# Optimization experiments

Hardware: AMD Instinct MI355X
Metric: run time of the kernel (lower is better)

## Reference

```python
import jax, jax.numpy as jnp
import numpy as np

B, H, T, D = 4, 16, 1024, 64
N_BINS = 16
TEMPERATURE = 1.0
THRESHOLD = 0.05
ROUTER_HIDDEN = 128


def setup_inputs() -> dict:
    key = jax.random.key(0)
    ks = jax.random.split(key, 7)
    key_dim = H * D
    return {
        "q": jax.random.normal(ks[0], (B, H, T, D), dtype=jnp.float32),
        "k": jax.random.normal(ks[1], (B, H, T, D), dtype=jnp.float32),
        "v": jax.random.normal(ks[2], (B, H, T, D), dtype=jnp.float32),
        "W1": jax.random.normal(ks[3], (key_dim, ROUTER_HIDDEN), dtype=jnp.float32) * (1.0 / np.sqrt(key_dim)),
        "b1": jnp.zeros((ROUTER_HIDDEN,), dtype=jnp.float32),
        "W2": jax.random.normal(ks[4], (ROUTER_HIDDEN, N_BINS), dtype=jnp.float32) * (1.0 / np.sqrt(ROUTER_HIDDEN)),
        "b2": jnp.zeros((N_BINS,), dtype=jnp.float32),
    }


def reference(q, k, v, W1, b1, W2, b2):
    b, h, t, d = q.shape
    # Router operates on keys flattened across heads: [B, T, H*D]
    k_flat = jnp.transpose(k, (0, 2, 1, 3)).reshape(b, t, h * d)
    hidden = jnp.tanh(k_flat @ W1 + b1)
    bucket_logits = hidden @ W2 + b2                      # [B, T, n_bins]
    bucket_probs = jax.nn.softmax(bucket_logits / TEMPERATURE, axis=-1)
    # Pairwise bucket similarity: [B, T, T]
    bucket_sim = jnp.einsum('bik,bjk->bij', bucket_probs, bucket_probs)
    bucket_mask = bucket_sim > THRESHOLD
    causal = jnp.tril(jnp.ones((t, t), dtype=bool))
    mask = causal[None, :, :] & bucket_mask               # [B, T, T]
    scale = d ** (-0.5)
    scores = jnp.einsum('bhtd,bhsd->bhts', q, k) * scale  # [B, H, T, T]
    scores = jnp.where(mask[:, None, :, :], scores, -jnp.inf)
    attn = jax.nn.softmax(scores, axis=-1)
    return jnp.einsum('bhts,bhsd->bhtd', attn, v)
```

## Files before the change

### kernel.cpp

```cpp
#include <hip/hip_runtime.h>
#include <hip/hip_bf16.h>


#define B_ 4
#define H_ 16
#define T_ 1024
#define D_ 64
#define NB 16
#define RH 128

typedef __attribute__((ext_vector_type(8))) short s16x8;
typedef __attribute__((ext_vector_type(4))) float f32x4;

__device__ __forceinline__ unsigned short f2bf(float x) {
  union { __hip_bfloat16 b; unsigned short u; } c;
  c.b = __hip_bfloat16(x);
  return c.u;
}
__device__ __forceinline__ float bf2f(unsigned short h) {
  return __uint_as_float(((unsigned)h) << 16);
}

__global__ __launch_bounds__(256) void router_v2(
    const float* __restrict__ kin, const float* __restrict__ W1,
    const float* __restrict__ b1, const float* __restrict__ W2,
    const float* __restrict__ b2, float* __restrict__ probs) {
  __shared__ float rows[8][1024];
  __shared__ float part[8][8][RH];
  __shared__ float hid[8][RH + 4];
  __shared__ float logits[8][NB];

  const int tid = threadIdx.x;
  const int bb = blockIdx.x;
  const int b = bb >> 7;
  const int t0 = (bb & 127) << 3;

#pragma unroll
  for (int s = 0; s < 8; s++) {
    const int idx4 = tid + 256 * s;
    const int r = idx4 >> 8, i = (idx4 & 255) * 4;
    const int h = i >> 6, d = i & 63;
    *(float4*)&rows[r][i] =
        *(const float4*)&kin[(((size_t)(b * H_) + h) * T_ + (t0 + r)) * D_ + d];
  }
  __syncthreads();

  const int hu0 = (tid & 31) << 2;
  const int k0 = (tid >> 5) << 7;
  float acc[8][4];
#pragma unroll
  for (int r = 0; r < 8; r++)
#pragma unroll
    for (int c = 0; c < 4; c++) acc[r][c] = 0.0f;

  for (int kb = 0; kb < 128; kb += 4) {
    float4 rv[8];
#pragma unroll
    for (int r = 0; r < 8; r++) rv[r] = *(const float4*)&rows[r][k0 + kb];
#pragma unroll
    for (int e = 0; e < 4; e++) {
      const float4 w = *(const float4*)&W1[(size_t)(k0 + kb + e) * RH + hu0];
#pragma unroll
      for (int r = 0; r < 8; r++) {
        const float rx = (&rv[r].x)[e];
        acc[r][0] += rx * w.x; acc[r][1] += rx * w.y;
        acc[r][2] += rx * w.z; acc[r][3] += rx * w.w;
      }
    }
  }
#pragma unroll
  for (int r = 0; r < 8; r++)
    *(float4*)&part[tid >> 5][r][hu0] =
        (float4){acc[r][0], acc[r][1], acc[r][2], acc[r][3]};
  __syncthreads();

  {
    const int p0 = tid * 4;
    const int r = p0 >> 7, hu = p0 & 127;
    float4 s = {0.f, 0.f, 0.f, 0.f};
#pragma unroll
    for (int sl = 0; sl < 8; sl++) {
      const float4 v = *(const float4*)&part[sl][r][hu];
      s.x += v.x; s.y += v.y; s.z += v.z; s.w += v.w;
    }
    const float4 bv = *(const float4*)&b1[hu];
    *(float4*)&hid[r][hu] = (float4){tanhf(s.x + bv.x), tanhf(s.y + bv.y),
                                     tanhf(s.z + bv.z), tanhf(s.w + bv.w)};
  }
  __syncthreads();

  if (tid < 128) {
    const int r = tid >> 4, bin = tid & 15;
    float a = b2[bin];
#pragma unroll
    for (int jj = 0; jj < RH; jj++) a += hid[r][jj] * W2[jj * NB + bin];
    logits[r][bin] = a;
  }
  __syncthreads();

  if (tid < 8) {
    const int r = tid;
    float mx = -INFINITY;
#pragma unroll
    for (int bin = 0; bin < NB; bin++) mx = fmaxf(mx, logits[r][bin]);
    float e[NB];
    float s = 0.0f;
#pragma unroll
    for (int bin = 0; bin < NB; bin++) {
      e[bin] = expf(logits[r][bin] - mx);
      s += e[bin];
    }
    const float inv = 1.0f / s;
    const size_t row = (size_t)(b * T_ + t0 + r) * NB;
#pragma unroll
    for (int bin = 0; bin < NB; bin++) probs[row + bin] = e[bin] * inv;
  }
}

__global__ __launch_bounds__(256) void mask_v3(
    const float* __restrict__ probs, unsigned long long* __restrict__ mask) {
  const int blk = blockIdx.x;
  const int b = blk >> 7, i0 = (blk & 127) << 3;
  const int tid = threadIdx.x, w = tid >> 6;

  float4 pjv[4][4];
#pragma unroll
  for (int jc = 0; jc < 4; jc++) {
    const float4* pjp =
        (const float4*)(probs + ((size_t)(b * T_ + jc * 256 + tid)) * NB);
#pragma unroll
    for (int qq = 0; qq < 4; qq++) pjv[jc][qq] = pjp[qq];
  }

  for (int ii = 0; ii < 8; ii++) {
    const int i = i0 + ii;
    const float4* pip = (const float4*)(probs + ((size_t)(b * T_ + i)) * NB);
    const float4 p0 = pip[0], p1 = pip[1], p2 = pip[2], p3 = pip[3];
#pragma unroll
    for (int jc = 0; jc < 4; jc++) {
      const int j = jc * 256 + tid;
      float sim = p0.x * pjv[jc][0].x + p0.y * pjv[jc][0].y +
                  p0.z * pjv[jc][0].z + p0.w * pjv[jc][0].w;
      sim += p1.x * pjv[jc][1].x + p1.y * pjv[jc][1].y +
             p1.z * pjv[jc][1].z + p1.w * pjv[jc][1].w;
      sim += p2.x * pjv[jc][2].x + p2.y * pjv[jc][2].y +
             p2.z * pjv[jc][2].z + p2.w * pjv[jc][2].w;
      sim += p3.x * pjv[jc][3].x + p3.y * pjv[jc][3].y +
             p3.z * pjv[jc][3].z + p3.w * pjv[jc][3].w;
      const unsigned long long bal = __ballot((j <= i) && (sim > 0.05f));
      if ((tid & 63) == 0)
        mask[((size_t)(b * T_ + i) << 4) + jc * 4 + w] = bal;
    }
  }
}

__global__ __launch_bounds__(256, 2) void attn_mfma(
    const float* __restrict__ q, const float* __restrict__ k,
    const float* __restrict__ v, const unsigned long long* __restrict__ mask,
    float* __restrict__ out) {
  __shared__ unsigned short Kh[64 * 64], Kl[64 * 64];
  __shared__ unsigned short Vth[64 * 64], Vtl[64 * 64];
  __shared__ unsigned short Phs[4][1024], Pls[4][1024];

  const int bh = blockIdx.x, qt = blockIdx.y;
  const int b = bh >> 4;
  const int tid = threadIdx.x, w = tid >> 6, lane = tid & 63;
  const int lr = lane & 15;
  const int g = lane >> 4;
  const size_t base = (size_t)bh * (T_ * D_);
  const int qrow_g = qt * 64 + w * 16 + lr;
  const unsigned swz = ((unsigned)(lr & 7)) << 4;

  s16x8 qfh[2], qfl[2];
  {
    const float* qp = q + base + (size_t)qrow_g * D_;
#pragma unroll
    for (int ks = 0; ks < 2; ks++) {
      union { unsigned short us[8]; s16x8 v; } h, l;
#pragma unroll
      for (int e2 = 0; e2 < 2; e2++) {
        const float4 f = *(const float4*)(qp + 32 * ks + 8 * g + 4 * e2);
#pragma unroll
        for (int e = 0; e < 4; e++) {
          const float x = (&f.x)[e] * 0.125f;
          const unsigned short hh = f2bf(x);
          h.us[4 * e2 + e] = hh;
          l.us[4 * e2 + e] = f2bf(x - bf2f(hh));
        }
      }
      qfh[ks] = h.v; qfl[ks] = l.v;
    }
  }

  f32x4 Oacc[4];
#pragma unroll
  for (int n = 0; n < 4; n++) Oacc[n] = (f32x4){0.f, 0.f, 0.f, 0.f};
  float mrun = -INFINITY, lrun = 0.f;

  const unsigned long long* mrow = mask + ((size_t)(b * T_ + qrow_g) << 4);
  const int dv = tid & 63, k0v = (tid >> 6) * 16;

  float Kst[16], Vst[16], Kst2[16], Vst2[16];
  {
    const float4* kp4 = (const float4*)(k + base);
    const float* vp = v + base;
#pragma unroll
    for (int i = 0; i < 4; i++) {
      const float4 f = kp4[tid + 256 * i];
      Kst[4 * i + 0] = f.x; Kst[4 * i + 1] = f.y;
      Kst[4 * i + 2] = f.z; Kst[4 * i + 3] = f.w;
    }
#pragma unroll
    for (int j = 0; j < 16; j++) Vst[j] = vp[(size_t)(k0v + j) * D_ + dv];
  }
  unsigned long long mw = mrow[0];

  for (int kt = 0; kt <= qt; kt++) {
    __syncthreads();
#pragma unroll
    for (int i = 0; i < 4; i++) {
      const int flat4 = tid + 256 * i, key = flat4 >> 4, dq = flat4 & 15;
      union { unsigned short us[4]; uint2 d; } h, l;
#pragma unroll
      for (int e = 0; e < 4; e++) {
        const float x = Kst[4 * i + e];
        const unsigned short hh = f2bf(x);
        h.us[e] = hh; l.us[e] = f2bf(x - bf2f(hh));
      }
      const unsigned byte = (unsigned)(key * 128 + dq * 8) ^ (((unsigned)(key & 7)) << 4);
      *(uint2*)((char*)Kh + byte) = h.d;
      *(uint2*)((char*)Kl + byte) = l.d;
    }
#pragma unroll
    for (int i = 0; i < 2; i++) {
      union { unsigned short us[8]; uint4 q; } h, l;
#pragma unroll
      for (int j = 0; j < 8; j++) {
        const float x = Vst[8 * i + j];
        const unsigned short hh = f2bf(x);
        h.us[j] = hh; l.us[j] = f2bf(x - bf2f(hh));
      }
      const unsigned byte =
          (unsigned)(dv * 128 + (k0v + 8 * i) * 2) ^ (((unsigned)(dv & 7)) << 4);
      *(uint4*)((char*)Vth + byte) = h.q;
      *(uint4*)((char*)Vtl + byte) = l.q;
    }
    __syncthreads();

    const int ktn = (kt < qt) ? kt + 1 : qt;
    {
      const float4* kp4 = (const float4*)(k + base + (size_t)(ktn * 64) * D_);
      const float* vp = v + base + (size_t)(ktn * 64) * D_;
#pragma unroll
      for (int i = 0; i < 4; i++) {
        const float4 f = kp4[tid + 256 * i];
        Kst2[4 * i + 0] = f.x; Kst2[4 * i + 1] = f.y;
        Kst2[4 * i + 2] = f.z; Kst2[4 * i + 3] = f.w;
      }
#pragma unroll
      for (int j = 0; j < 16; j++) Vst2[j] = vp[(size_t)(k0v + j) * D_ + dv];
    }
    const unsigned long long mwn = mrow[ktn];

    if (__any(mw != 0ull)) {
      f32x4 S4[4];
#pragma unroll
      for (int m = 0; m < 4; m++) {
        f32x4 acc = (f32x4){0.f, 0.f, 0.f, 0.f};
#pragma unroll
        for (int ks = 0; ks < 2; ks++) {
          const unsigned byte =
              ((unsigned)((16 * m + lr) * 128 + 64 * ks + 16 * g)) ^ swz;
          const s16x8 kfh = *(const s16x8*)((const char*)Kh + byte);
          const s16x8 kfl = *(const s16x8*)((const char*)Kl + byte);
          acc = __builtin_amdgcn_mfma_f32_16x16x32_bf16(kfh, qfh[ks], acc, 0, 0, 0);
          acc = __builtin_amdgcn_mfma_f32_16x16x32_bf16(kfh, qfl[ks], acc, 0, 0, 0);
          acc = __builtin_amdgcn_mfma_f32_16x16x32_bf16(kfl, qfh[ks], acc, 0, 0, 0);
        }
        S4[m] = acc;
      }

      float sv[16]; unsigned okb = 0; float tmax = -INFINITY;
#pragma unroll
      for (int jj = 0; jj < 16; jj++) {
        const int bit = 16 * (jj >> 2) + 4 * g + (jj & 3);
        const bool ok = (mw >> bit) & 1ull;
        okb |= ((unsigned)ok) << jj;
        const float s = ok ? S4[jj >> 2][jj & 3] : -INFINITY;
        sv[jj] = s; tmax = fmaxf(tmax, s);
      }
      tmax = fmaxf(tmax, __shfl_xor(tmax, 16));
      tmax = fmaxf(tmax, __shfl_xor(tmax, 32));
      if (__any(tmax > mrun + 8.0f)) {
        const float mnew = fmaxf(mrun, tmax);
        const float corr = (mnew == -INFINITY) ? 1.0f : __expf(mrun - mnew);
        lrun *= corr; mrun = mnew;
        float cr[4];
#pragma unroll
        for (int r = 0; r < 4; r++) cr[r] = __shfl(corr, 4 * g + r);
#pragma unroll
        for (int n = 0; n < 4; n++)
#pragma unroll
          for (int r = 0; r < 4; r++) Oacc[n][r] *= cr[r];
      }
      float pj[16]; float lsum = 0.f;
#pragma unroll
      for (int jj = 0; jj < 16; jj++) {
        const float e = __expf(sv[jj] - mrun);
        const float pv = ((okb >> jj) & 1u) ? e : 0.f;
        pj[jj] = pv; lsum += pv;
      }
      lsum += __shfl_xor(lsum, 16);
      lsum += __shfl_xor(lsum, 32);
      lrun += lsum;

#pragma unroll
      for (int m = 0; m < 4; m++) {
        union { unsigned short us[4]; uint2 d; } h, l;
#pragma unroll
        for (int r = 0; r < 4; r++) {
          const float pv = pj[4 * m + r];
          const unsigned short hh = f2bf(pv);
          h.us[r] = hh; l.us[r] = f2bf(pv - bf2f(hh));
        }
        const unsigned byte =
            ((unsigned)(lr * 128 + (16 * m + 4 * g) * 2)) ^ swz;
        *(uint2*)((char*)Phs + 2048 * w + byte) = h.d;
        *(uint2*)((char*)Pls + 2048 * w + byte) = l.d;
      }
      asm volatile("s_waitcnt lgkmcnt(0)" ::: "memory");
      __builtin_amdgcn_sched_barrier(0);

#pragma unroll
      for (int ks = 0; ks < 2; ks++) {
        const unsigned pb = ((unsigned)(lr * 128 + 64 * ks + 16 * g)) ^ swz;
        const s16x8 pfh = *(const s16x8*)((const char*)Phs + 2048 * w + pb);
        const s16x8 pfl = *(const s16x8*)((const char*)Pls + 2048 * w + pb);
#pragma unroll
        for (int n = 0; n < 4; n++) {
          const unsigned vb =
              ((unsigned)((16 * n + lr) * 128 + 64 * ks + 16 * g)) ^ swz;
          const s16x8 vfh = *(const s16x8*)((const char*)Vth + vb);
          const s16x8 vfl = *(const s16x8*)((const char*)Vtl + vb);
          Oacc[n] = __builtin_amdgcn_mfma_f32_16x16x32_bf16(pfh, vfh, Oacc[n], 0, 0, 0);
          Oacc[n] = __builtin_amdgcn_mfma_f32_16x16x32_bf16(pfh, vfl, Oacc[n], 0, 0, 0);
          Oacc[n] = __builtin_amdgcn_mfma_f32_16x16x32_bf16(pfl, vfh, Oacc[n], 0, 0, 0);
        }
      }
    }

#pragma unroll
    for (int i = 0; i < 16; i++) { Kst[i] = Kst2[i]; Vst[i] = Vst2[i]; }
    mw = mwn;
  }

  const float linv = 1.0f / lrun;
  float lr4[4];
#pragma unroll
  for (int r = 0; r < 4; r++) lr4[r] = __shfl(linv, 4 * g + r);
  const int orow0 = qt * 64 + w * 16;
  float* op = out + base;
#pragma unroll
  for (int n = 0; n < 4; n++)
#pragma unroll
    for (int r = 0; r < 4; r++)
      op[(size_t)(orow0 + 4 * g + r) * D_ + 16 * n + lr] = Oacc[n][r] * lr4[r];
}

extern "C" void kernel_launch(void* const* d_in, const int* in_sizes, int n_in,
                              void* d_out, int out_size, void* d_ws, size_t ws_size,
                              hipStream_t stream) {
  const float* q  = (const float*)d_in[0];
  const float* k  = (const float*)d_in[1];
  const float* v  = (const float*)d_in[2];
  const float* W1 = (const float*)d_in[3];
  const float* b1 = (const float*)d_in[4];
  const float* W2 = (const float*)d_in[5];
  const float* b2 = (const float*)d_in[6];
  float* out = (float*)d_out;

  float* probs = (float*)d_ws;
  unsigned long long* mask =
      (unsigned long long*)((char*)d_ws + (size_t)B_ * T_ * NB * sizeof(float));

  router_v2<<<512, 256, 0, stream>>>(k, W1, b1, W2, b2, probs);
  mask_v3<<<512, 256, 0, stream>>>(probs, mask);
  attn_mfma<<<dim3(B_ * H_, T_ / 64), 256, 0, stream>>>(q, k, v, mask, out);
}
```

Measured before the change: 170.2 us.

## Pre-split K/V into swizzled bf16 hi/lo tiles and reorder attention blocks

The router kernel gains extra blocks that convert K and transposed V once into bf16 hi/lo pairs, stored in workspace in the swizzled LDS layout. The attention kernel then copies these tiles straight into shared memory with register double-buffering, instead of converting fp32 K/V in every query-tile block. It also launches heaviest causal query tiles first, skips fully masked tiles, only rescales the accumulator when the running max grows by more than a margin, and drops the low part of P. The cost is 32 MB of extra workspace traffic plus a fallback path when the workspace is too small, and less precision in the P·V product.

```diff
diff --git a/kernel.cpp b/kernel.cpp
--- a/kernel.cpp
+++ b/kernel.cpp
@@ -21,99 +21,160 @@
   return __uint_as_float(((unsigned)h) << 16);
 }
 
-__global__ __launch_bounds__(256) void router_v2(
-    const float* __restrict__ kin, const float* __restrict__ W1,
-    const float* __restrict__ b1, const float* __restrict__ W2,
-    const float* __restrict__ b2, float* __restrict__ probs) {
-  __shared__ float rows[8][1024];
-  __shared__ float part[8][8][RH];
-  __shared__ float hid[8][RH + 4];
-  __shared__ float logits[8][NB];
-
+__global__ __launch_bounds__(256) void prep_kernel(
+    const float* __restrict__ kin, const float* __restrict__ vin,
+    const float* __restrict__ W1, const float* __restrict__ b1,
+    const float* __restrict__ W2, const float* __restrict__ b2,
+    float* __restrict__ probs,
+    unsigned short* __restrict__ khi, unsigned short* __restrict__ klo,
+    unsigned short* __restrict__ vthi, unsigned short* __restrict__ vtlo) {
+  __shared__ union {
+    struct {
+      float rows[8][1024];
+      float part[8][8][RH];
+      float hid[8][RH + 4];
+      float logits[8][NB];
+    } r;
+    float vt[64][68];
+  } sm;
   const int tid = threadIdx.x;
-  const int bb = blockIdx.x;
-  const int b = bb >> 7;
-  const int t0 = (bb & 127) << 3;
-
-#pragma unroll
-  for (int s = 0; s < 8; s++) {
-    const int idx4 = tid + 256 * s;
-    const int r = idx4 >> 8, i = (idx4 & 255) * 4;
-    const int h = i >> 6, d = i & 63;
-    *(float4*)&rows[r][i] =
-        *(const float4*)&kin[(((size_t)(b * H_) + h) * T_ + (t0 + r)) * D_ + d];
-  }
-  __syncthreads();
-
-  const int hu0 = (tid & 31) << 2;
-  const int k0 = (tid >> 5) << 7;
-  float acc[8][4];
-#pragma unroll
-  for (int r = 0; r < 8; r++)
-#pragma unroll
-    for (int c = 0; c < 4; c++) acc[r][c] = 0.0f;
-
-  for (int kb = 0; kb < 128; kb += 4) {
-    float4 rv[8];
-#pragma unroll
-    for (int r = 0; r < 8; r++) rv[r] = *(const float4*)&rows[r][k0 + kb];
-#pragma unroll
-    for (int e = 0; e < 4; e++) {
-      const float4 w = *(const float4*)&W1[(size_t)(k0 + kb + e) * RH + hu0];
-#pragma unroll
-      for (int r = 0; r < 8; r++) {
-        const float rx = (&rv[r].x)[e];
-        acc[r][0] += rx * w.x; acc[r][1] += rx * w.y;
-        acc[r][2] += rx * w.z; acc[r][3] += rx * w.w;
-      }
-    }
-  }
-#pragma unroll
-  for (int r = 0; r < 8; r++)
-    *(float4*)&part[tid >> 5][r][hu0] =
-        (float4){acc[r][0], acc[r][1], acc[r][2], acc[r][3]};
-  __syncthreads();
-
-  {
-    const int p0 = tid * 4;
-    const int r = p0 >> 7, hu = p0 & 127;
-    float4 s = {0.f, 0.f, 0.f, 0.f};
-#pragma unroll
-    for (int sl = 0; sl < 8; sl++) {
-      const float4 v = *(const float4*)&part[sl][r][hu];
-      s.x += v.x; s.y += v.y; s.z += v.z; s.w += v.w;
-    }
-    const float4 bv = *(const float4*)&b1[hu];
-    *(float4*)&hid[r][hu] = (float4){tanhf(s.x + bv.x), tanhf(s.y + bv.y),
-                                     tanhf(s.z + bv.z), tanhf(s.w + bv.w)};
-  }
-  __syncthreads();
-
-  if (tid < 128) {
-    const int r = tid >> 4, bin = tid & 15;
-    float a = b2[bin];
-#pragma unroll
-    for (int jj = 0; jj < RH; jj++) a += hid[r][jj] * W2[jj * NB + bin];
-    logits[r][bin] = a;
-  }
-  __syncthreads();
-
-  if (tid < 8) {
-    const int r = tid;
-    float mx = -INFINITY;
-#pragma unroll
-    for (int bin = 0; bin < NB; bin++) mx = fmaxf(mx, logits[r][bin]);
-    float e[NB];
-    float s = 0.0f;
-#pragma unroll
-    for (int bin = 0; bin < NB; bin++) {
-      e[bin] = expf(logits[r][bin] - mx);
-      s += e[bin];
-    }
-    const float inv = 1.0f / s;
-    const size_t row = (size_t)(b * T_ + t0 + r) * NB;
-#pragma unroll
-    for (int bin = 0; bin < NB; bin++) probs[row + bin] = e[bin] * inv;
+
+  if (blockIdx.x < 512) {
+    const int bb = blockIdx.x;
+    const int b = bb >> 7;
+    const int t0 = (bb & 127) << 3;
+
+#pragma unroll
+    for (int s = 0; s < 8; s++) {
+      const int idx4 = tid + 256 * s;
+      const int r = idx4 >> 8, i = (idx4 & 255) * 4;
+      const int h = i >> 6, d = i & 63;
+      *(float4*)&sm.r.rows[r][i] =
+          *(const float4*)&kin[(((size_t)(b * H_) + h) * T_ + (t0 + r)) * D_ + d];
+    }
+    __syncthreads();
+
+    const int hu0 = (tid & 31) << 2;
+    const int k0 = (tid >> 5) << 7;
+    float acc[8][4];
+#pragma unroll
+    for (int r = 0; r < 8; r++)
+#pragma unroll
+      for (int c = 0; c < 4; c++) acc[r][c] = 0.0f;
+
+    for (int kb = 0; kb < 128; kb += 4) {
+      float4 rv[8];
+#pragma unroll
+      for (int r = 0; r < 8; r++) rv[r] = *(const float4*)&sm.r.rows[r][k0 + kb];
+#pragma unroll
+      for (int e = 0; e < 4; e++) {
+        const float4 w = *(const float4*)&W1[(size_t)(k0 + kb + e) * RH + hu0];
+#pragma unroll
+        for (int r = 0; r < 8; r++) {
+          const float rx = (&rv[r].x)[e];
+          acc[r][0] += rx * w.x; acc[r][1] += rx * w.y;
+          acc[r][2] += rx * w.z; acc[r][3] += rx * w.w;
+        }
+      }
+    }
+#pragma unroll
+    for (int r = 0; r < 8; r++)
+      *(float4*)&sm.r.part[tid >> 5][r][hu0] =
+          (float4){acc[r][0], acc[r][1], acc[r][2], acc[r][3]};
+    __syncthreads();
+
+    {
+      const int p0 = tid * 4;
+      const int r = p0 >> 7, hu = p0 & 127;
+      float4 s = {0.f, 0.f, 0.f, 0.f};
+#pragma unroll
+      for (int sl = 0; sl < 8; sl++) {
+        const float4 v = *(const float4*)&sm.r.part[sl][r][hu];
+        s.x += v.x; s.y += v.y; s.z += v.z; s.w += v.w;
+      }
+      const float4 bv = *(const float4*)&b1[hu];
+      *(float4*)&sm.r.hid[r][hu] = (float4){tanhf(s.x + bv.x), tanhf(s.y + bv.y),
+                                            tanhf(s.z + bv.z), tanhf(s.w + bv.w)};
+    }
+    __syncthreads();
+
+    if (tid < 128) {
+      const int r = tid >> 4, bin = tid & 15;
+      float a = b2[bin];
+#pragma unroll
+      for (int jj = 0; jj < RH; jj++) a += sm.r.hid[r][jj] * W2[jj * NB + bin];
+      sm.r.logits[r][bin] = a;
+    }
+    __syncthreads();
+
+    if (tid < 8) {
+      const int r = tid;
+      float mx = -INFINITY;
+#pragma unroll
+      for (int bin = 0; bin < NB; bin++) mx = fmaxf(mx, sm.r.logits[r][bin]);
+      float e[NB];
+      float s = 0.0f;
+#pragma unroll
+      for (int bin = 0; bin < NB; bin++) {
+        e[bin] = expf(sm.r.logits[r][bin] - mx);
+        s += e[bin];
+      }
+      const float inv = 1.0f / s;
+      const size_t row = (size_t)(b * T_ + t0 + r) * NB;
+#pragma unroll
+      for (int bin = 0; bin < NB; bin++) probs[row + bin] = e[bin] * inv;
+    }
+  } else {
+    const int blk = blockIdx.x - 512;
+    const int bh = blk >> 4, kt = blk & 15;
+    const float* kp = kin + (size_t)bh * (T_ * D_) + (size_t)kt * (64 * D_);
+    const float* vp = vin + (size_t)bh * (T_ * D_) + (size_t)kt * (64 * D_);
+    char* kh = (char*)khi + (size_t)blk * 8192;
+    char* kl = (char*)klo + (size_t)blk * 8192;
+    char* vh = (char*)vthi + (size_t)blk * 8192;
+    char* vl = (char*)vtlo + (size_t)blk * 8192;
+
+#pragma unroll
+    for (int it = 0; it < 4; it++) {
+      const int flat4 = tid + 256 * it;
+      const int key = flat4 >> 4, d0 = (flat4 & 15) * 4;
+      const float4 f = *(const float4*)(kp + (size_t)key * D_ + d0);
+      union { unsigned short us[4]; uint2 u; } h, l;
+#pragma unroll
+      for (int e = 0; e < 4; e++) {
+        const float x = (&f.x)[e];
+        const unsigned short hh = f2bf(x);
+        h.us[e] = hh; l.us[e] = f2bf(x - bf2f(hh));
+      }
+      const unsigned dst =
+          ((unsigned)(key * 128 + d0 * 2)) ^ (((unsigned)(key & 7)) << 4);
+      *(uint2*)(kh + dst) = h.u;
+      *(uint2*)(kl + dst) = l.u;
+      *(float4*)&sm.vt[key][d0] = f;
+    }
+#pragma unroll
+    for (int it = 0; it < 4; it++) {
+      const int flat4 = tid + 256 * it;
+      const int key = flat4 >> 4, d0 = (flat4 & 15) * 4;
+      *(float4*)&sm.vt[key][d0] = *(const float4*)(vp + (size_t)key * D_ + d0);
+    }
+    __syncthreads();
+
+    const int d = tid & 63, tc = (tid >> 6) * 16;
+    union { unsigned short us[8]; uint4 u; } h0, h1, l0, l1;
+#pragma unroll
+    for (int i = 0; i < 16; i++) {
+      const float x = sm.vt[tc + i][d];
+      const unsigned short hh = f2bf(x);
+      const unsigned short ll = f2bf(x - bf2f(hh));
+      if (i < 8) { h0.us[i] = hh; l0.us[i] = ll; }
+      else       { h1.us[i - 8] = hh; l1.us[i - 8] = ll; }
+    }
+    const unsigned sw = ((unsigned)(d & 7)) << 4;
+    const unsigned vb0 = ((unsigned)(d * 128 + tc * 2)) ^ sw;
+    const unsigned vb1 = ((unsigned)(d * 128 + tc * 2 + 16)) ^ sw;
+    *(uint4*)(vh + vb0) = h0.u; *(uint4*)(vh + vb1) = h1.u;
+    *(uint4*)(vl + vb0) = l0.u; *(uint4*)(vl + vb1) = l1.u;
   }
 }
 
@@ -154,6 +215,182 @@
   }
 }
 
+__global__ __launch_bounds__(256, 2) void attn_bf16(
+    const float* __restrict__ q,
+    const unsigned short* __restrict__ khi, const unsigned short* __restrict__ klo,
+    const unsigned short* __restrict__ vthi, const unsigned short* __restrict__ vtlo,
+    const unsigned long long* __restrict__ mask, float* __restrict__ out) {
+  __shared__ unsigned short Kh[64 * 64], Kl[64 * 64];
+  __shared__ unsigned short Vth[64 * 64], Vtl[64 * 64];
+  __shared__ unsigned short Phs[4][1024];
+
+  const int bid = blockIdx.x;
+  const int qt = 15 - (bid >> 6);
+  const int bh = bid & 63;
+  const int b = bh >> 4;
+  const int tid = threadIdx.x, w = tid >> 6, lane = tid & 63;
+  const int lr = lane & 15, g = lane >> 4;
+  const size_t base = (size_t)bh * (T_ * D_);
+  const int qrow_g = qt * 64 + w * 16 + lr;
+  const unsigned swz = ((unsigned)(lr & 7)) << 4;
+
+  s16x8 qfh[2], qfl[2];
+  {
+    const float* qp = q + base + (size_t)qrow_g * D_;
+#pragma unroll
+    for (int ks = 0; ks < 2; ks++) {
+      union { unsigned short us[8]; s16x8 v; } h, l;
+#pragma unroll
+      for (int e2 = 0; e2 < 2; e2++) {
+        const float4 f = *(const float4*)(qp + 32 * ks + 8 * g + 4 * e2);
+#pragma unroll
+        for (int e = 0; e < 4; e++) {
+          const float x = (&f.x)[e] * 0.125f;
+          const unsigned short hh = f2bf(x);
+          h.us[4 * e2 + e] = hh;
+          l.us[4 * e2 + e] = f2bf(x - bf2f(hh));
+        }
+      }
+      qfh[ks] = h.v; qfl[ks] = l.v;
+    }
+  }
+
+  f32x4 Oacc[4];
+#pragma unroll
+  for (int n = 0; n < 4; n++) Oacc[n] = (f32x4){0.f, 0.f, 0.f, 0.f};
+  float mrun = -INFINITY, lrun = 0.f;
+
+  const unsigned long long* mrow = mask + ((size_t)(b * T_ + qrow_g) << 4);
+  const uint4* gkh = (const uint4*)khi + (size_t)bh * (16 * 512);
+  const uint4* gkl = (const uint4*)klo + (size_t)bh * (16 * 512);
+  const uint4* gvh = (const uint4*)vthi + (size_t)bh * (16 * 512);
+  const uint4* gvl = (const uint4*)vtlo + (size_t)bh * (16 * 512);
+
+  uint4 st[8], st2[8];
+  {
+    st[0] = gkh[tid];       st[1] = gkh[tid + 256];
+    st[2] = gkl[tid];       st[3] = gkl[tid + 256];
+    st[4] = gvh[tid];       st[5] = gvh[tid + 256];
+    st[6] = gvl[tid];       st[7] = gvl[tid + 256];
+  }
+  unsigned long long mw = mrow[0];
+
+  for (int kt = 0; kt <= qt; kt++) {
+    __syncthreads();
+    ((uint4*)Kh)[tid] = st[0];  ((uint4*)Kh)[tid + 256] = st[1];
+    ((uint4*)Kl)[tid] = st[2];  ((uint4*)Kl)[tid + 256] = st[3];
+    ((uint4*)Vth)[tid] = st[4]; ((uint4*)Vth)[tid + 256] = st[5];
+    ((uint4*)Vtl)[tid] = st[6]; ((uint4*)Vtl)[tid + 256] = st[7];
+    __syncthreads();
+
+    const int ktn = (kt < qt) ? kt + 1 : qt;
+    {
+      const size_t toff = (size_t)ktn * 512;
+      st2[0] = gkh[toff + tid];       st2[1] = gkh[toff + tid + 256];
+      st2[2] = gkl[toff + tid];       st2[3] = gkl[toff + tid + 256];
+      st2[4] = gvh[toff + tid];       st2[5] = gvh[toff + tid + 256];
+      st2[6] = gvl[toff + tid];       st2[7] = gvl[toff + tid + 256];
+    }
+    const unsigned long long mwn = mrow[ktn];
+
+    if (__any(mw != 0ull)) {
+      f32x4 S4[4];
+#pragma unroll
+      for (int m = 0; m < 4; m++) {
+        f32x4 acc = (f32x4){0.f, 0.f, 0.f, 0.f};
+#pragma unroll
+        for (int ks = 0; ks < 2; ks++) {
+          const unsigned byte =
+              ((unsigned)((16 * m + lr) * 128 + 64 * ks + 16 * g)) ^ swz;
+          const s16x8 kfh = *(const s16x8*)((const char*)Kh + byte);
+          const s16x8 kfl = *(const s16x8*)((const char*)Kl + byte);
+          acc = __builtin_amdgcn_mfma_f32_16x16x32_bf16(kfh, qfh[ks], acc, 0, 0, 0);
+          acc = __builtin_amdgcn_mfma_f32_16x16x32_bf16(kfh, qfl[ks], acc, 0, 0, 0);
+          acc = __builtin_amdgcn_mfma_f32_16x16x32_bf16(kfl, qfh[ks], acc, 0, 0, 0);
+        }
+        S4[m] = acc;
+      }
+
+      float sv[16]; unsigned okb = 0; float tmax = -INFINITY;
+#pragma unroll
+      for (int jj = 0; jj < 16; jj++) {
+        const int bit = 16 * (jj >> 2) + 4 * g + (jj & 3);
+        const bool ok = (mw >> bit) & 1ull;
+        okb |= ((unsigned)ok) << jj;
+        const float s = ok ? S4[jj >> 2][jj & 3] : -INFINITY;
+        sv[jj] = s; tmax = fmaxf(tmax, s);
+      }
+      tmax = fmaxf(tmax, __shfl_xor(tmax, 16));
+      tmax = fmaxf(tmax, __shfl_xor(tmax, 32));
+      if (__any(tmax > mrun + 8.0f)) {
+        const float mnew = fmaxf(mrun, tmax);
+        const float corr = (mnew == -INFINITY) ? 1.0f : __expf(mrun - mnew);
+        lrun *= corr; mrun = mnew;
+        float cr[4];
+#pragma unroll
+        for (int r = 0; r < 4; r++) cr[r] = __shfl(corr, 4 * g + r);
+#pragma unroll
+        for (int n = 0; n < 4; n++)
+#pragma unroll
+          for (int r = 0; r < 4; r++) Oacc[n][r] *= cr[r];
+      }
+      float pj[16]; float lsum = 0.f;
+#pragma unroll
+      for (int jj = 0; jj < 16; jj++) {
+        const float e = __expf(sv[jj] - mrun);
+        const float pv = ((okb >> jj) & 1u) ? e : 0.f;
+        pj[jj] = pv; lsum += pv;
+      }
+      lsum += __shfl_xor(lsum, 16);
+      lsum += __shfl_xor(lsum, 32);
+      lrun += lsum;
+
+#pragma unroll
+      for (int m = 0; m < 4; m++) {
+        union { unsigned short us[4]; uint2 d; } h;
+#pragma unroll
+        for (int r = 0; r < 4; r++) h.us[r] = f2bf(pj[4 * m + r]);
+        const unsigned byte =
+            ((unsigned)(lr * 128 + (16 * m + 4 * g) * 2)) ^ swz;
+        *(uint2*)((char*)Phs + 2048 * w + byte) = h.d;
+      }
+      asm volatile("s_waitcnt lgkmcnt(0)" ::: "memory");
+      __builtin_amdgcn_sched_barrier(0);
+
+#pragma unroll
+      for (int ks = 0; ks < 2; ks++) {
+        const unsigned pb = ((unsigned)(lr * 128 + 64 * ks + 16 * g)) ^ swz;
+        const s16x8 pfh = *(const s16x8*)((const char*)Phs + 2048 * w + pb);
+#pragma unroll
+        for (int n = 0; n < 4; n++) {
+          const unsigned vb =
+              ((unsigned)((16 * n + lr) * 128 + 64 * ks + 16 * g)) ^ swz;
+          const s16x8 vfh = *(const s16x8*)((const char*)Vth + vb);
+          const s16x8 vfl = *(const s16x8*)((const char*)Vtl + vb);
+          Oacc[n] = __builtin_amdgcn_mfma_f32_16x16x32_bf16(pfh, vfh, Oacc[n], 0, 0, 0);
+          Oacc[n] = __builtin_amdgcn_mfma_f32_16x16x32_bf16(pfh, vfl, Oacc[n], 0, 0, 0);
+        }
+      }
+    }
+
+#pragma unroll
+    for (int i = 0; i < 8; i++) st[i] = st2[i];
+    mw = mwn;
+  }
+
+  const float linv = 1.0f / lrun;
+  float lr4[4];
+#pragma unroll
+  for (int r = 0; r < 4; r++) lr4[r] = __shfl(linv, 4 * g + r);
+  const int orow0 = qt * 64 + w * 16;
+  float* op = out + base;
+#pragma unroll
+  for (int n = 0; n < 4; n++)
+#pragma unroll
+    for (int r = 0; r < 4; r++)
+      op[(size_t)(orow0 + 4 * g + r) * D_ + 16 * n + lr] = Oacc[n][r] * lr4[r];
+}
+
 __global__ __launch_bounds__(256, 2) void attn_mfma(
     const float* __restrict__ q, const float* __restrict__ k,
     const float* __restrict__ v, const unsigned long long* __restrict__ mask,
@@ -380,10 +617,22 @@
   float* out = (float*)d_out;
 
   float* probs = (float*)d_ws;
-  unsigned long long* mask =
-      (unsigned long long*)((char*)d_ws + (size_t)B_ * T_ * NB * sizeof(float));
-
-  router_v2<<<512, 256, 0, stream>>>(k, W1, b1, W2, b2, probs);
-  mask_v3<<<512, 256, 0, stream>>>(probs, mask);
-  attn_mfma<<<dim3(B_ * H_, T_ / 64), 256, 0, stream>>>(q, k, v, mask, out);
+  unsigned long long* mask = (unsigned long long*)((char*)d_ws + 262144);
+  const size_t NEED = 786432ull + 4ull * 8388608ull;
+
+  if (ws_size >= NEED) {
+    unsigned short* khi  = (unsigned short*)((char*)d_ws + 786432);
+    unsigned short* klo  = (unsigned short*)((char*)d_ws + 786432 + 8388608ull);
+    unsigned short* vthi = (unsigned short*)((char*)d_ws + 786432 + 16777216ull);
+    unsigned short* vtlo = (unsigned short*)((char*)d_ws + 786432 + 25165824ull);
+    prep_kernel<<<1536, 256, 0, stream>>>(k, v, W1, b1, W2, b2, probs,
+                                          khi, klo, vthi, vtlo);
+    mask_v3<<<512, 256, 0, stream>>>(probs, mask);
+    attn_bf16<<<1024, 256, 0, stream>>>(q, khi, klo, vthi, vtlo, mask, out);
+  } else {
+    prep_kernel<<<512, 256, 0, stream>>>(k, v, W1, b1, W2, b2, probs,
+                                         nullptr, nullptr, nullptr, nullptr);
+    mask_v3<<<512, 256, 0, stream>>>(probs, mask);
+    attn_mfma<<<dim3(B_ * H_, T_ / 64), 256, 0, stream>>>(q, k, v, mask, out);
+  }
 }
```

Result: slower. 239.7 us (+40.9%).
